# Kernel tuning notes

Hardware: AMD Instinct MI355X
Metric: run time of the kernel (lower is better)

## Reference

```python
import jax, jax.numpy as jnp
import numpy as np

H = 4        # no_heads
CH = 32      # per-head hidden (c_hidden)
INF = 1.0e9

def setup_inputs() -> dict:
    key = jax.random.key(0)
    ks = jax.random.split(key, 8)
    B, I, J, C = 1, 256, 256, 128
    s = 0.02
    return {
        "x": jax.random.normal(ks[0], (B, I, J, C), jnp.float32),
        "mask": jnp.ones((B, I, J), jnp.float32),
        "chunk_size": 0,
        "ln_w": jnp.ones((C,), jnp.float32),
        "ln_b": jnp.zeros((C,), jnp.float32),
        "w_tri": jax.random.normal(ks[1], (C, H), jnp.float32) * s,
        "wq": jax.random.normal(ks[2], (C, H * CH), jnp.float32) * s,
        "wk": jax.random.normal(ks[3], (C, H * CH), jnp.float32) * s,
        "wv": jax.random.normal(ks[4], (C, H * CH), jnp.float32) * s,
        "wg": jax.random.normal(ks[5], (C, H * CH), jnp.float32) * s,
        "bg": jnp.zeros((H * CH,), jnp.float32),
        "wo": jax.random.normal(ks[6], (H * CH, C), jnp.float32) * s,
        "bo": jnp.zeros((C,), jnp.float32),
    }

def _layer_norm(x, w, b, eps=1e-5):
    mu = jnp.mean(x, axis=-1, keepdims=True)
    var = jnp.mean(jnp.square(x - mu), axis=-1, keepdims=True)
    return (x - mu) * jax.lax.rsqrt(var + eps) * w + b

def reference(x, mask, chunk_size, ln_w, ln_b, w_tri, wq, wk, wv, wg, bg, wo, bo):
    # starting=True -> no transpose of (I, J)
    B, I, J, C = x.shape
    xn = _layer_norm(x, ln_w, ln_b)                                   # [B,I,J,C]
    # biases
    mask_bias = (INF * (mask - 1.0))[:, :, None, None, :]             # [B,I,1,1,J]
    tri_bias = jnp.einsum("bijc,ch->bhij", xn, w_tri)[:, None]        # [B,1,H,I,J]
    # gated multi-head attention over the J axis (per row I)
    q = (xn @ wq).reshape(B, I, J, H, CH) * (CH ** -0.5)              # [B,I,J,H,CH]
    k = (xn @ wk).reshape(B, I, J, H, CH)
    v = (xn @ wv).reshape(B, I, J, H, CH)
    scores = jnp.einsum("biqhd,bikhd->bihqk", q, k) + mask_bias + tri_bias
    a = jax.nn.softmax(scores, axis=-1)                               # [B,I,H,J,J]
    o = jnp.einsum("bihqk,bikhd->biqhd", a, v)                        # [B,I,J,H,CH]
    g = jax.nn.sigmoid(xn @ wg + bg).reshape(B, I, J, H, CH)
    o = (o * g).reshape(B, I, J, H * CH)
    return o @ wo + bo                                                # [B,I,J,C]
```

## Files before the change

kernel.cpp:

```cpp
#include <hip/hip_runtime.h>
#include <math.h>

#define NI 256
#define NJ 256
#define NC 128
#define NH 4
#define NCH 32
#define TOKS ((long)NI * NJ)

typedef __attribute__((ext_vector_type(8)))  __bf16        bf16x8;
typedef __attribute__((ext_vector_type(8)))  unsigned short u16x8;
typedef __attribute__((ext_vector_type(4)))  unsigned int   u32x4;
typedef __attribute__((ext_vector_type(16))) float         f32x16;

__device__ __forceinline__ unsigned short f2bf(float f) {
    unsigned u = __builtin_bit_cast(unsigned, f);
    u += 0x7fffu + ((u >> 16) & 1u);
    return (unsigned short)(u >> 16);
}
__device__ __forceinline__ float bf2f(unsigned short s) {
    return __builtin_bit_cast(float, ((unsigned)s) << 16);
}
__device__ __forceinline__ float exp2_fast(float x) {
    float r;
    asm("v_exp_f32 %0, %1" : "=v"(r) : "v"(x));
    return r;
}
__device__ __forceinline__ f32x16 fzero16() {
    f32x16 z;
#pragma unroll
    for (int r = 0; r < 16; ++r) z[r] = 0.f;
    return z;
}
__device__ __forceinline__ f32x16 mfma16(bf16x8 a, bf16x8 b, f32x16 c) {
    return __builtin_amdgcn_mfma_f32_32x32x16_bf16(a, b, c, 0, 0, 0);
}

#define LOG2E 1.4426950408889634f

__global__ __launch_bounds__(256) void convert_weights(
    const float* __restrict__ wq, const float* __restrict__ wk,
    const float* __restrict__ wv, const float* __restrict__ wg,
    const float* __restrict__ wo, const float* __restrict__ w_tri,
    unsigned short* __restrict__ Wt_all, unsigned short* __restrict__ Wto,
    unsigned short* __restrict__ Wtri_pad)
{
    int id = blockIdx.x * 256 + threadIdx.x;
    if (id < 4 * 16384) {
        int m = id >> 14, r = id & 16383;
        int kk = r >> 7, c = r & 127;
        const float* W = (m == 0) ? wq : (m == 1) ? wk : (m == 2) ? wv : wg;
        Wt_all[(m * 128 + c) * 128 + kk] = f2bf(W[kk * 128 + c]);
    } else if (id < 5 * 16384) {
        int r = id - 4 * 16384;
        int kk = r >> 7, c = r & 127;
        Wto[c * 128 + kk] = f2bf(wo[kk * 128 + c]);
    } else {
        int r = id - 5 * 16384;
        int col = r >> 7, kk = r & 127;
        Wtri_pad[col * 128 + kk] = (col < NH) ? f2bf(w_tri[kk * NH + col] * LOG2E)
                                              : (unsigned short)0;
    }
}

#define XNP 136
__global__ __launch_bounds__(256, 2) void ln_proj_mfma(
    const float* __restrict__ x, const float* __restrict__ ln_w, const float* __restrict__ ln_b,
    const unsigned short* __restrict__ Wt_all, const unsigned short* __restrict__ Wtri_pad,
    const float* __restrict__ bg,
    unsigned short* __restrict__ q, unsigned short* __restrict__ k,
    unsigned short* __restrict__ v, unsigned short* __restrict__ g,
    float* __restrict__ tswz)
{
    __shared__ unsigned short xn[64 * XNP];
    const int tid = threadIdx.x;
    const long tok0 = (long)blockIdx.x * 64;

    const int lane8 = tid & 7;
#pragma unroll
    for (int p = 0; p < 2; ++p) {
        const int t = p * 32 + (tid >> 3);
        const float4* xrow = (const float4*)(x + (tok0 + t) * NC + lane8 * 16);
        float4 xv[4];
        float s = 0.f;
#pragma unroll
        for (int u = 0; u < 4; ++u) {
            xv[u] = xrow[u];
            s += xv[u].x + xv[u].y + xv[u].z + xv[u].w;
        }
#pragma unroll
        for (int off = 4; off; off >>= 1) s += __shfl_down(s, off, 8);
        const float mu = __shfl(s, 0, 8) * (1.f / (float)NC);
        float s2 = 0.f;
#pragma unroll
        for (int u = 0; u < 4; ++u) {
            float dx;
            dx = xv[u].x - mu; s2 += dx * dx;
            dx = xv[u].y - mu; s2 += dx * dx;
            dx = xv[u].z - mu; s2 += dx * dx;
            dx = xv[u].w - mu; s2 += dx * dx;
        }
#pragma unroll
        for (int off = 4; off; off >>= 1) s2 += __shfl_down(s2, off, 8);
        const float rstd = rsqrtf(__shfl(s2, 0, 8) * (1.f / (float)NC) + 1e-5f);
#pragma unroll
        for (int u = 0; u < 4; ++u) {
            const int c = lane8 * 16 + u * 4;
            const float4 lw = *(const float4*)(ln_w + c);
            const float4 lb = *(const float4*)(ln_b + c);
            float o0 = (xv[u].x - mu) * rstd * lw.x + lb.x;
            float o1 = (xv[u].y - mu) * rstd * lw.y + lb.y;
            float o2 = (xv[u].z - mu) * rstd * lw.z + lb.z;
            float o3 = (xv[u].w - mu) * rstd * lw.w + lb.w;
            unsigned p0 = (unsigned)f2bf(o0) | ((unsigned)f2bf(o1) << 16);
            unsigned p1 = (unsigned)f2bf(o2) | ((unsigned)f2bf(o3) << 16);
            *(unsigned*)&xn[t * XNP + c]     = p0;
            *(unsigned*)&xn[t * XNP + c + 2] = p1;
        }
    }
    __syncthreads();

    const int w = tid >> 6, L = tid & 63, lh = L >> 5, lc = L & 31;
    f32x16 acc[2][4], accT[2];
#pragma unroll
    for (int mt = 0; mt < 2; ++mt) {
        accT[mt] = fzero16();
#pragma unroll
        for (int nt = 0; nt < 4; ++nt) acc[mt][nt] = fzero16();
    }

#pragma unroll
    for (int k0 = 0; k0 < 8; ++k0) {
        bf16x8 a0 = *(const bf16x8*)&xn[(lc)      * XNP + k0 * 16 + lh * 8];
        bf16x8 a1 = *(const bf16x8*)&xn[(32 + lc) * XNP + k0 * 16 + lh * 8];
#pragma unroll
        for (int nt = 0; nt < 4; ++nt) {
            const int ntile = w + 4 * nt;
            bf16x8 b = *(const bf16x8*)&Wt_all[(ntile * 32 + lc) * 128 + k0 * 16 + lh * 8];
            acc[0][nt] = mfma16(a0, b, acc[0][nt]);
            acc[1][nt] = mfma16(a1, b, acc[1][nt]);
        }
        bf16x8 bt = *(const bf16x8*)&Wtri_pad[lc * 128 + k0 * 16 + lh * 8];
        accT[0] = mfma16(a0, bt, accT[0]);
        accT[1] = mfma16(a1, bt, accT[1]);
    }

    const int a_row = (int)(tok0 >> 8);
    const int b0    = (int)(tok0 & 255);
    int rowl[16];
#pragma unroll
    for (int r = 0; r < 16; ++r) rowl[r] = (r & 3) + 8 * (r >> 2) + 4 * lh;

    if (lc < NH) {
        const int qt_i = a_row >> 5;
        const int lsw  = ((a_row & 31) + 32 * lh) * 16;
#pragma unroll
        for (int mt = 0; mt < 2; ++mt) {
            float* dst = tswz + ((long)((lc * 8 + qt_i) * 8 + (b0 >> 5) + mt)) * 1024 + lsw;
#pragma unroll
            for (int u = 0; u < 4; ++u)
                *(float4*)(dst + u * 4) = make_float4(accT[mt][4*u],   accT[mt][4*u+1],
                                                      accT[mt][4*u+2], accT[mt][4*u+3]);
        }
    }

    const float bgv = bg[w * 32 + lc];
#pragma unroll
    for (int nt = 0; nt < 4; ++nt) {
        unsigned short* O = (nt == 0) ? q : (nt == 1) ? k : (nt == 2) ? v : g;
        __syncthreads();
#pragma unroll
        for (int mt = 0; mt < 2; ++mt) {
#pragma unroll
            for (int r = 0; r < 16; ++r) {
                const int row = mt * 32 + rowl[r];
                float val = acc[mt][nt][r];
                if (nt == 0) val *= 0.25503486f;
                if (nt == 3) val = __builtin_amdgcn_rcpf(1.f + __expf(-(val + bgv)));
                xn[row * XNP + w * 32 + lc] = f2bf(val);
            }
        }
        __syncthreads();
#pragma unroll
        for (int it = 0; it < 4; ++it) {
            const int row = tid >> 2, cc = (tid & 3) * 8;
            *(u16x8*)(O + (((long)a_row * NH + it) * NJ + b0 + row) * NCH + cc) =
                *(const u16x8*)&xn[row * XNP + it * 32 + cc];
        }
    }
}

#define KSP 40
#define VTP 264
#define OSP 36
__global__ __launch_bounds__(256, 2) void attn_fused(
    const unsigned short* __restrict__ q, const unsigned short* __restrict__ k,
    const unsigned short* __restrict__ v, const unsigned short* __restrict__ g,
    const float* __restrict__ tswz, const float* __restrict__ mask,
    const unsigned short* __restrict__ Wto, const float* __restrict__ bo,
    float* __restrict__ out)
{
    __shared__ char smem[75776];
    float* maskb = (float*)(smem + 74752);
    float* outs  = (float*)smem;

    const int i = blockIdx.x, qh = blockIdx.y;
    const int tid = threadIdx.x;
    const int w = tid >> 6, L = tid & 63, lh = L >> 5, lc = L & 31;
    const int qt = qh * 4 + w;
    const int qrow = qt * 32 + lc;

    maskb[tid] = (1.0e9f * LOG2E) * (mask[i * NJ + tid] - 1.0f);

    bf16x8 kreg[4];
    u16x8  vreg[4];
    {
        const long base0 = (long)i * NH * NJ * NCH;
#pragma unroll
        for (int it = 0; it < 4; ++it) {
            const int idx = it * 256 + tid;
            const int key = idx >> 2, c8 = (idx & 3) * 8;
            kreg[it] = *(const bf16x8*)(k + base0 + key * NCH + c8);
        }
#pragma unroll
        for (int u = 0; u < 4; ++u)
            vreg[u] = *(const u16x8*)(v + base0 + (long)tid * NCH + u * 8);
    }

    f32x16 outacc[4];
#pragma unroll
    for (int ct = 0; ct < 4; ++ct) outacc[ct] = fzero16();

#pragma unroll
    for (int h = 0; h < NH; ++h) {
        unsigned short* Ks = (unsigned short*)(smem + (h & 1) * 20480);
        unsigned short* Vt = (unsigned short*)(smem + 40960 + (h & 1) * 16896);
        const long base = ((long)i * NH + h) * NJ * NCH;

        if (h) __syncthreads();
#pragma unroll
        for (int it = 0; it < 4; ++it) {
            const int idx = it * 256 + tid;
            const int key = idx >> 2, c8 = (idx & 3) * 8;
            *(bf16x8*)&Ks[key * KSP + c8] = kreg[it];
        }
#pragma unroll
        for (int u = 0; u < 8; ++u) {
            Vt[(u)      * VTP + tid] = vreg[0][u];
            Vt[(u + 8)  * VTP + tid] = vreg[1][u];
            Vt[(u + 16) * VTP + tid] = vreg[2][u];
            Vt[(u + 24) * VTP + tid] = vreg[3][u];
        }
        __syncthreads();

        if (h < NH - 1) {
            const long basen = base + (long)NJ * NCH;
#pragma unroll
            for (int it = 0; it < 4; ++it) {
                const int idx = it * 256 + tid;
                const int key = idx >> 2, c8 = (idx & 3) * 8;
                kreg[it] = *(const bf16x8*)(k + basen + key * NCH + c8);
            }
#pragma unroll
            for (int u = 0; u < 4; ++u)
                vreg[u] = *(const u16x8*)(v + basen + (long)tid * NCH + u * 8);
        }

        const bf16x8 a0 = *(const bf16x8*)(q + base + (long)qrow * NCH + lh * 8);
        const bf16x8 a1 = *(const bf16x8*)(q + base + (long)qrow * NCH + 16 + lh * 8);
        ushort4 gv[4];
#pragma unroll
        for (int gg = 0; gg < 4; ++gg)
            gv[gg] = *(const ushort4*)(g + base + (long)qrow * NCH + gg * 8 + 4 * lh);
        const float* tbase = tswz + ((long)(h * 8 + qt) * 8) * 1024 + (long)L * 16;

        float ls = 0.f;
        f32x16 O = fzero16();

#pragma unroll
        for (int t = 0; t < 8; ++t) {
            bf16x8 kb0 = *(const bf16x8*)&Ks[(t * 32 + lc) * KSP + lh * 8];
            bf16x8 kb1 = *(const bf16x8*)&Ks[(t * 32 + lc) * KSP + 16 + lh * 8];
            f32x16 s = fzero16();
            s = mfma16(kb0, a0, s);
            s = mfma16(kb1, a1, s);

            unsigned pk[8];
            const float* tv = tbase + (long)t * 1024;
#pragma unroll
            for (int gg = 0; gg < 4; ++gg) {
                const float4 tb = *(const float4*)(tv + gg * 4);
                const float4 mb = *(const float4*)&maskb[t * 32 + gg * 8 + 4 * lh];
                const float p0 = exp2_fast(fminf(s[4 * gg + 0] + tb.x + mb.x, 43.4f));
                const float p1 = exp2_fast(fminf(s[4 * gg + 1] + tb.y + mb.y, 43.4f));
                const float p2 = exp2_fast(fminf(s[4 * gg + 2] + tb.z + mb.z, 43.4f));
                const float p3 = exp2_fast(fminf(s[4 * gg + 3] + tb.w + mb.w, 43.4f));
                ls += (p0 + p1) + (p2 + p3);
                pk[2 * gg]     = (unsigned)f2bf(p0) | ((unsigned)f2bf(p1) << 16);
                pk[2 * gg + 1] = (unsigned)f2bf(p2) | ((unsigned)f2bf(p3) << 16);
            }

#pragma unroll
            for (int ss = 0; ss < 2; ++ss) {
                const unsigned give0 = lh ? pk[4 * ss]     : pk[4 * ss + 2];
                const unsigned give1 = lh ? pk[4 * ss + 1] : pk[4 * ss + 3];
                const unsigned t0 = __shfl_xor(give0, 32);
                const unsigned t1 = __shfl_xor(give1, 32);
                u32x4 bw;
                bw[0] = lh ? t0 : pk[4 * ss];
                bw[1] = lh ? t1 : pk[4 * ss + 1];
                bw[2] = lh ? pk[4 * ss + 2] : t0;
                bw[3] = lh ? pk[4 * ss + 3] : t1;
                const bf16x8 pb = __builtin_bit_cast(bf16x8, bw);
                const bf16x8 va = *(const bf16x8*)&Vt[lc * VTP + t * 32 + ss * 16 + lh * 8];
                O = mfma16(va, pb, O);
            }
        }

        ls += __shfl_xor(ls, 32);
        const float rl = __builtin_amdgcn_rcpf(ls);
        unsigned pk2[8];
#pragma unroll
        for (int gg = 0; gg < 4; ++gg) {
            const float o0 = O[4 * gg + 0] * rl * bf2f(gv[gg].x);
            const float o1 = O[4 * gg + 1] * rl * bf2f(gv[gg].y);
            const float o2 = O[4 * gg + 2] * rl * bf2f(gv[gg].z);
            const float o3 = O[4 * gg + 3] * rl * bf2f(gv[gg].w);
            pk2[2 * gg]     = (unsigned)f2bf(o0) | ((unsigned)f2bf(o1) << 16);
            pk2[2 * gg + 1] = (unsigned)f2bf(o2) | ((unsigned)f2bf(o3) << 16);
        }

#pragma unroll
        for (int ss = 0; ss < 2; ++ss) {
            const unsigned give0 = lh ? pk2[4 * ss]     : pk2[4 * ss + 2];
            const unsigned give1 = lh ? pk2[4 * ss + 1] : pk2[4 * ss + 3];
            const unsigned t0 = __shfl_xor(give0, 32);
            const unsigned t1 = __shfl_xor(give1, 32);
            u32x4 bw;
            bw[0] = lh ? t0 : pk2[4 * ss];
            bw[1] = lh ? t1 : pk2[4 * ss + 1];
            bw[2] = lh ? pk2[4 * ss + 2] : t0;
            bw[3] = lh ? pk2[4 * ss + 3] : t1;
            const bf16x8 ogb = __builtin_bit_cast(bf16x8, bw);
#pragma unroll
            for (int ct = 0; ct < 4; ++ct) {
                const bf16x8 wa = *(const bf16x8*)&Wto[(ct * 32 + lc) * 128 + h * 32 + ss * 16 + lh * 8];
                outacc[ct] = mfma16(wa, ogb, outacc[ct]);
            }
        }
    }

    int rowl[16];
#pragma unroll
    for (int r = 0; r < 16; ++r) rowl[r] = (r & 3) + 8 * (r >> 2) + 4 * lh;
#pragma unroll
    for (int ct = 0; ct < 4; ++ct) {
        __syncthreads();
#pragma unroll
        for (int r = 0; r < 16; ++r)
            outs[(w * 32 + lc) * OSP + rowl[r]] = outacc[ct][r];
        __syncthreads();
#pragma unroll
        for (int it = 0; it < 4; ++it) {
            const int fi = it * 256 + tid;
            const int row = fi >> 3, c4 = fi & 7;
            const float4 vv = *(const float4*)&outs[row * OSP + c4 * 4];
            const float4 bo4 = *(const float4*)(bo + ct * 32 + c4 * 4);
            float4 st;
            st.x = vv.x + bo4.x; st.y = vv.y + bo4.y;
            st.z = vv.z + bo4.z; st.w = vv.w + bo4.w;
            *(float4*)(out + ((long)i * NJ + qh * 128 + row) * NC + ct * 32 + c4 * 4) = st;
        }
    }
}

extern "C" void kernel_launch(void* const* d_in, const int* in_sizes, int n_in,
                              void* d_out, int out_size, void* d_ws, size_t ws_size,
                              hipStream_t stream) {
    const float* x     = (const float*)d_in[0];
    const float* mask  = (const float*)d_in[1];
    const float* ln_w  = (const float*)d_in[3];
    const float* ln_b  = (const float*)d_in[4];
    const float* w_tri = (const float*)d_in[5];
    const float* wq    = (const float*)d_in[6];
    const float* wk    = (const float*)d_in[7];
    const float* wv    = (const float*)d_in[8];
    const float* wg    = (const float*)d_in[9];
    const float* bg    = (const float*)d_in[10];
    const float* wo    = (const float*)d_in[11];
    const float* bo    = (const float*)d_in[12];
    float* out = (float*)d_out;

    char* p = (char*)d_ws;
    const long QB  = TOKS * NC * sizeof(unsigned short);
    unsigned short* q  = (unsigned short*)p; p += QB;
    unsigned short* k  = (unsigned short*)p; p += QB;
    unsigned short* v  = (unsigned short*)p; p += QB;
    unsigned short* g  = (unsigned short*)p; p += QB;
    float* tswz = (float*)p; p += (long)NH * NI * NJ * sizeof(float);
    unsigned short* Wt_all   = (unsigned short*)p; p += 4 * 128 * 128 * sizeof(unsigned short);
    unsigned short* Wto      = (unsigned short*)p; p += 128 * 128 * sizeof(unsigned short);
    unsigned short* Wtri_pad = (unsigned short*)p; p += 32 * 128 * sizeof(unsigned short);

    hipLaunchKernelGGL(convert_weights, dim3(336), dim3(256), 0, stream,
                       wq, wk, wv, wg, wo, w_tri, Wt_all, Wto, Wtri_pad);
    hipLaunchKernelGGL(ln_proj_mfma, dim3(TOKS / 64), dim3(256), 0, stream,
                       x, ln_w, ln_b, Wt_all, Wtri_pad, bg, q, k, v, g, tswz);
    hipLaunchKernelGGL(attn_fused, dim3(NI, 2), dim3(256), 0, stream,
                       q, k, v, g, tswz, mask, Wto, bo, out);
}
```

Measured before the change: 173.2 us.

## Process two heads per pass in attention kernel and use permlane32 swaps

The attention kernel now stages K/V for two heads at once into both shared-memory buffers and interleaves their QK, softmax and PV MFMA chains. This halves the number of block barriers and gives the scheduler independent work to hide MFMA and exp latency. The cross-half shuffles via __shfl_xor are replaced with v_permlane32_swap_b32 inline asm, including the row-sum reduction. The cost is higher register pressure from double K/V prefetch registers and two accumulators, which could spill or cut occupancy under launch_bounds(256,2).

```diff
diff --git a/kernel.cpp b/kernel.cpp
--- a/kernel.cpp
+++ b/kernel.cpp
@@ -25,6 +25,12 @@
     float r;
     asm("v_exp_f32 %0, %1" : "=v"(r) : "v"(x));
     return r;
+}
+__device__ __forceinline__ void permswap(unsigned &a, unsigned &b) {
+    asm volatile("v_permlane32_swap_b32 %0, %1" : "+v"(a), "+v"(b));
+}
+__device__ __forceinline__ void permswapf(float &a, float &b) {
+    asm volatile("v_permlane32_swap_b32 %0, %1" : "+v"(a), "+v"(b));
 }
 __device__ __forceinline__ f32x16 fzero16() {
     f32x16 z;
@@ -201,6 +207,10 @@
     float* __restrict__ out)
 {
     __shared__ char smem[75776];
+    unsigned short* Ks0 = (unsigned short*)smem;
+    unsigned short* Ks1 = (unsigned short*)(smem + 20480);
+    unsigned short* Vt0 = (unsigned short*)(smem + 40960);
+    unsigned short* Vt1 = (unsigned short*)(smem + 40960 + 16896);
     float* maskb = (float*)(smem + 74752);
     float* outs  = (float*)smem;
 
@@ -212,142 +222,177 @@
 
     maskb[tid] = (1.0e9f * LOG2E) * (mask[i * NJ + tid] - 1.0f);
 
-    bf16x8 kreg[4];
-    u16x8  vreg[4];
-    {
-        const long base0 = (long)i * NH * NJ * NCH;
+    const int kidx = tid >> 2, kc8 = (tid & 3) * 8;
+    const long rowbase = (long)i * NH * NJ * NCH;
+
+    bf16x8 kregA[4], kregB[4];
+    u16x8  vregA[4], vregB[4];
+#pragma unroll
+    for (int it = 0; it < 4; ++it) {
+        const int idx = it * 256 + tid;
+        const int key = idx >> 2, c8 = (idx & 3) * 8;
+        kregA[it] = *(const bf16x8*)(k + rowbase + key * NCH + c8);
+        kregB[it] = *(const bf16x8*)(k + rowbase + (long)NJ * NCH + key * NCH + c8);
+    }
+#pragma unroll
+    for (int u = 0; u < 4; ++u) {
+        vregA[u] = *(const u16x8*)(v + rowbase + (long)tid * NCH + u * 8);
+        vregB[u] = *(const u16x8*)(v + rowbase + (long)NJ * NCH + (long)tid * NCH + u * 8);
+    }
+
+    f32x16 outacc[4];
+#pragma unroll
+    for (int ct = 0; ct < 4; ++ct) outacc[ct] = fzero16();
+
+#pragma unroll
+    for (int hp = 0; hp < 2; ++hp) {
+        const int h0 = 2 * hp, h1 = 2 * hp + 1;
+        const long baseA = ((long)i * NH + h0) * NJ * NCH;
+        const long baseB = ((long)i * NH + h1) * NJ * NCH;
+
 #pragma unroll
         for (int it = 0; it < 4; ++it) {
             const int idx = it * 256 + tid;
             const int key = idx >> 2, c8 = (idx & 3) * 8;
-            kreg[it] = *(const bf16x8*)(k + base0 + key * NCH + c8);
-        }
-#pragma unroll
-        for (int u = 0; u < 4; ++u)
-            vreg[u] = *(const u16x8*)(v + base0 + (long)tid * NCH + u * 8);
-    }
-
-    f32x16 outacc[4];
-#pragma unroll
-    for (int ct = 0; ct < 4; ++ct) outacc[ct] = fzero16();
-
-#pragma unroll
-    for (int h = 0; h < NH; ++h) {
-        unsigned short* Ks = (unsigned short*)(smem + (h & 1) * 20480);
-        unsigned short* Vt = (unsigned short*)(smem + 40960 + (h & 1) * 16896);
-        const long base = ((long)i * NH + h) * NJ * NCH;
-
-        if (h) __syncthreads();
-#pragma unroll
-        for (int it = 0; it < 4; ++it) {
-            const int idx = it * 256 + tid;
-            const int key = idx >> 2, c8 = (idx & 3) * 8;
-            *(bf16x8*)&Ks[key * KSP + c8] = kreg[it];
+            *(bf16x8*)&Ks0[key * KSP + c8] = kregA[it];
+            *(bf16x8*)&Ks1[key * KSP + c8] = kregB[it];
         }
 #pragma unroll
         for (int u = 0; u < 8; ++u) {
-            Vt[(u)      * VTP + tid] = vreg[0][u];
-            Vt[(u + 8)  * VTP + tid] = vreg[1][u];
-            Vt[(u + 16) * VTP + tid] = vreg[2][u];
-            Vt[(u + 24) * VTP + tid] = vreg[3][u];
-        }
+            Vt0[(u)      * VTP + tid] = vregA[0][u];
+            Vt0[(u + 8)  * VTP + tid] = vregA[1][u];
+            Vt0[(u + 16) * VTP + tid] = vregA[2][u];
+            Vt0[(u + 24) * VTP + tid] = vregA[3][u];
+            Vt1[(u)      * VTP + tid] = vregB[0][u];
+            Vt1[(u + 8)  * VTP + tid] = vregB[1][u];
+            Vt1[(u + 16) * VTP + tid] = vregB[2][u];
+            Vt1[(u + 24) * VTP + tid] = vregB[3][u];
+        }
+
+        const bf16x8 aA0 = *(const bf16x8*)(q + baseA + (long)qrow * NCH + lh * 8);
+        const bf16x8 aA1 = *(const bf16x8*)(q + baseA + (long)qrow * NCH + 16 + lh * 8);
+        const bf16x8 aB0 = *(const bf16x8*)(q + baseB + (long)qrow * NCH + lh * 8);
+        const bf16x8 aB1 = *(const bf16x8*)(q + baseB + (long)qrow * NCH + 16 + lh * 8);
+        const float* tbA = tswz + ((long)(h0 * 8 + qt) * 8) * 1024 + (long)L * 16;
+        const float* tbB = tswz + ((long)(h1 * 8 + qt) * 8) * 1024 + (long)L * 16;
+
         __syncthreads();
 
-        if (h < NH - 1) {
-            const long basen = base + (long)NJ * NCH;
+        float lsA = 0.f, lsB = 0.f;
+        f32x16 O0 = fzero16(), O1 = fzero16();
+
+#pragma unroll
+        for (int t = 0; t < 8; ++t) {
+            const int krow = (t * 32 + lc) * KSP;
+            bf16x8 ka0 = *(const bf16x8*)&Ks0[krow + lh * 8];
+            bf16x8 ka1 = *(const bf16x8*)&Ks0[krow + 16 + lh * 8];
+            bf16x8 kb0 = *(const bf16x8*)&Ks1[krow + lh * 8];
+            bf16x8 kb1 = *(const bf16x8*)&Ks1[krow + 16 + lh * 8];
+            f32x16 s0 = fzero16(), s1 = fzero16();
+            s0 = mfma16(ka0, aA0, s0);
+            s1 = mfma16(kb0, aB0, s1);
+            s0 = mfma16(ka1, aA1, s0);
+            s1 = mfma16(kb1, aB1, s1);
+
+            unsigned pkA[8], pkB[8];
+            const float* tvA = tbA + (long)t * 1024;
+            const float* tvB = tbB + (long)t * 1024;
+#pragma unroll
+            for (int gg = 0; gg < 4; ++gg) {
+                const float4 mb  = *(const float4*)&maskb[t * 32 + gg * 8 + 4 * lh];
+                const float4 tba = *(const float4*)(tvA + gg * 4);
+                const float4 tbb = *(const float4*)(tvB + gg * 4);
+                const float a0 = exp2_fast(fminf(s0[4*gg+0] + tba.x + mb.x, 43.4f));
+                const float a1 = exp2_fast(fminf(s0[4*gg+1] + tba.y + mb.y, 43.4f));
+                const float a2 = exp2_fast(fminf(s0[4*gg+2] + tba.z + mb.z, 43.4f));
+                const float a3 = exp2_fast(fminf(s0[4*gg+3] + tba.w + mb.w, 43.4f));
+                const float b0_ = exp2_fast(fminf(s1[4*gg+0] + tbb.x + mb.x, 43.4f));
+                const float b1_ = exp2_fast(fminf(s1[4*gg+1] + tbb.y + mb.y, 43.4f));
+                const float b2_ = exp2_fast(fminf(s1[4*gg+2] + tbb.z + mb.z, 43.4f));
+                const float b3_ = exp2_fast(fminf(s1[4*gg+3] + tbb.w + mb.w, 43.4f));
+                lsA += (a0 + a1) + (a2 + a3);
+                lsB += (b0_ + b1_) + (b2_ + b3_);
+                pkA[2*gg]   = (unsigned)f2bf(a0)  | ((unsigned)f2bf(a1)  << 16);
+                pkA[2*gg+1] = (unsigned)f2bf(a2)  | ((unsigned)f2bf(a3)  << 16);
+                pkB[2*gg]   = (unsigned)f2bf(b0_) | ((unsigned)f2bf(b1_) << 16);
+                pkB[2*gg+1] = (unsigned)f2bf(b2_) | ((unsigned)f2bf(b3_) << 16);
+            }
+
+#pragma unroll
+            for (int ss = 0; ss < 2; ++ss) {
+                unsigned x0 = pkA[4*ss], x1 = pkA[4*ss+1], x2 = pkA[4*ss+2], x3 = pkA[4*ss+3];
+                permswap(x0, x2); permswap(x1, x3);
+                u32x4 bwA; bwA[0] = x0; bwA[1] = x1; bwA[2] = x2; bwA[3] = x3;
+                const bf16x8 pbA = __builtin_bit_cast(bf16x8, bwA);
+                const bf16x8 vaA = *(const bf16x8*)&Vt0[lc * VTP + t * 32 + ss * 16 + lh * 8];
+                O0 = mfma16(vaA, pbA, O0);
+
+                unsigned y0 = pkB[4*ss], y1 = pkB[4*ss+1], y2 = pkB[4*ss+2], y3 = pkB[4*ss+3];
+                permswap(y0, y2); permswap(y1, y3);
+                u32x4 bwB; bwB[0] = y0; bwB[1] = y1; bwB[2] = y2; bwB[3] = y3;
+                const bf16x8 pbB = __builtin_bit_cast(bf16x8, bwB);
+                const bf16x8 vaB = *(const bf16x8*)&Vt1[lc * VTP + t * 32 + ss * 16 + lh * 8];
+                O1 = mfma16(vaB, pbB, O1);
+            }
+        }
+
+        if (hp == 0) {
+            const long nA = rowbase + 2L * NJ * NCH;
+            const long nB = rowbase + 3L * NJ * NCH;
 #pragma unroll
             for (int it = 0; it < 4; ++it) {
                 const int idx = it * 256 + tid;
                 const int key = idx >> 2, c8 = (idx & 3) * 8;
-                kreg[it] = *(const bf16x8*)(k + basen + key * NCH + c8);
-            }
-#pragma unroll
-            for (int u = 0; u < 4; ++u)
-                vreg[u] = *(const u16x8*)(v + basen + (long)tid * NCH + u * 8);
-        }
-
-        const bf16x8 a0 = *(const bf16x8*)(q + base + (long)qrow * NCH + lh * 8);
-        const bf16x8 a1 = *(const bf16x8*)(q + base + (long)qrow * NCH + 16 + lh * 8);
-        ushort4 gv[4];
-#pragma unroll
-        for (int gg = 0; gg < 4; ++gg)
-            gv[gg] = *(const ushort4*)(g + base + (long)qrow * NCH + gg * 8 + 4 * lh);
-        const float* tbase = tswz + ((long)(h * 8 + qt) * 8) * 1024 + (long)L * 16;
-
-        float ls = 0.f;
-        f32x16 O = fzero16();
-
-#pragma unroll
-        for (int t = 0; t < 8; ++t) {
-            bf16x8 kb0 = *(const bf16x8*)&Ks[(t * 32 + lc) * KSP + lh * 8];
-            bf16x8 kb1 = *(const bf16x8*)&Ks[(t * 32 + lc) * KSP + 16 + lh * 8];
-            f32x16 s = fzero16();
-            s = mfma16(kb0, a0, s);
-            s = mfma16(kb1, a1, s);
-
-            unsigned pk[8];
-            const float* tv = tbase + (long)t * 1024;
+                kregA[it] = *(const bf16x8*)(k + nA + key * NCH + c8);
+                kregB[it] = *(const bf16x8*)(k + nB + key * NCH + c8);
+            }
+#pragma unroll
+            for (int u = 0; u < 4; ++u) {
+                vregA[u] = *(const u16x8*)(v + nA + (long)tid * NCH + u * 8);
+                vregB[u] = *(const u16x8*)(v + nB + (long)tid * NCH + u * 8);
+            }
+        }
+
+#pragma unroll
+        for (int hs = 0; hs < 2; ++hs) {
+            const long base = hs ? baseB : baseA;
+            const int h = hs ? h1 : h0;
+            f32x16& O = hs ? O1 : O0;
+            float la = hs ? lsB : lsA, lb = la;
+            permswapf(la, lb);
+            const float rl = __builtin_amdgcn_rcpf(la + lb);
+
+            ushort4 gv[4];
+#pragma unroll
+            for (int gg = 0; gg < 4; ++gg)
+                gv[gg] = *(const ushort4*)(g + base + (long)qrow * NCH + gg * 8 + 4 * lh);
+
+            unsigned pk2[8];
 #pragma unroll
             for (int gg = 0; gg < 4; ++gg) {
-                const float4 tb = *(const float4*)(tv + gg * 4);
-                const float4 mb = *(const float4*)&maskb[t * 32 + gg * 8 + 4 * lh];
-                const float p0 = exp2_fast(fminf(s[4 * gg + 0] + tb.x + mb.x, 43.4f));
-                const float p1 = exp2_fast(fminf(s[4 * gg + 1] + tb.y + mb.y, 43.4f));
-                const float p2 = exp2_fast(fminf(s[4 * gg + 2] + tb.z + mb.z, 43.4f));
-                const float p3 = exp2_fast(fminf(s[4 * gg + 3] + tb.w + mb.w, 43.4f));
-                ls += (p0 + p1) + (p2 + p3);
-                pk[2 * gg]     = (unsigned)f2bf(p0) | ((unsigned)f2bf(p1) << 16);
-                pk[2 * gg + 1] = (unsigned)f2bf(p2) | ((unsigned)f2bf(p3) << 16);
+                const float o0 = O[4*gg+0] * rl * bf2f(gv[gg].x);
+                const float o1 = O[4*gg+1] * rl * bf2f(gv[gg].y);
+                const float o2 = O[4*gg+2] * rl * bf2f(gv[gg].z);
+                const float o3 = O[4*gg+3] * rl * bf2f(gv[gg].w);
+                pk2[2*gg]   = (unsigned)f2bf(o0) | ((unsigned)f2bf(o1) << 16);
+                pk2[2*gg+1] = (unsigned)f2bf(o2) | ((unsigned)f2bf(o3) << 16);
             }
 
 #pragma unroll
             for (int ss = 0; ss < 2; ++ss) {
-                const unsigned give0 = lh ? pk[4 * ss]     : pk[4 * ss + 2];
-                const unsigned give1 = lh ? pk[4 * ss + 1] : pk[4 * ss + 3];
-                const unsigned t0 = __shfl_xor(give0, 32);
-                const unsigned t1 = __shfl_xor(give1, 32);
-                u32x4 bw;
-                bw[0] = lh ? t0 : pk[4 * ss];
-                bw[1] = lh ? t1 : pk[4 * ss + 1];
-                bw[2] = lh ? pk[4 * ss + 2] : t0;
-                bw[3] = lh ? pk[4 * ss + 3] : t1;
-                const bf16x8 pb = __builtin_bit_cast(bf16x8, bw);
-                const bf16x8 va = *(const bf16x8*)&Vt[lc * VTP + t * 32 + ss * 16 + lh * 8];
-                O = mfma16(va, pb, O);
-            }
-        }
-
-        ls += __shfl_xor(ls, 32);
-        const float rl = __builtin_amdgcn_rcpf(ls);
-        unsigned pk2[8];
-#pragma unroll
-        for (int gg = 0; gg < 4; ++gg) {
-            const float o0 = O[4 * gg + 0] * rl * bf2f(gv[gg].x);
-            const float o1 = O[4 * gg + 1] * rl * bf2f(gv[gg].y);
-            const float o2 = O[4 * gg + 2] * rl * bf2f(gv[gg].z);
-            const float o3 = O[4 * gg + 3] * rl * bf2f(gv[gg].w);
-            pk2[2 * gg]     = (unsigned)f2bf(o0) | ((unsigned)f2bf(o1) << 16);
-            pk2[2 * gg + 1] = (unsigned)f2bf(o2) | ((unsigned)f2bf(o3) << 16);
-        }
-
-#pragma unroll
-        for (int ss = 0; ss < 2; ++ss) {
-            const unsigned give0 = lh ? pk2[4 * ss]     : pk2[4 * ss + 2];
-            const unsigned give1 = lh ? pk2[4 * ss + 1] : pk2[4 * ss + 3];
-            const unsigned t0 = __shfl_xor(give0, 32);
-            const unsigned t1 = __shfl_xor(give1, 32);
-            u32x4 bw;
-            bw[0] = lh ? t0 : pk2[4 * ss];
-            bw[1] = lh ? t1 : pk2[4 * ss + 1];
-            bw[2] = lh ? pk2[4 * ss + 2] : t0;
-            bw[3] = lh ? pk2[4 * ss + 3] : t1;
-            const bf16x8 ogb = __builtin_bit_cast(bf16x8, bw);
-#pragma unroll
-            for (int ct = 0; ct < 4; ++ct) {
-                const bf16x8 wa = *(const bf16x8*)&Wto[(ct * 32 + lc) * 128 + h * 32 + ss * 16 + lh * 8];
-                outacc[ct] = mfma16(wa, ogb, outacc[ct]);
-            }
-        }
+                unsigned x0 = pk2[4*ss], x1 = pk2[4*ss+1], x2 = pk2[4*ss+2], x3 = pk2[4*ss+3];
+                permswap(x0, x2); permswap(x1, x3);
+                u32x4 bw; bw[0] = x0; bw[1] = x1; bw[2] = x2; bw[3] = x3;
+                const bf16x8 ogb = __builtin_bit_cast(bf16x8, bw);
+#pragma unroll
+                for (int ct = 0; ct < 4; ++ct) {
+                    const bf16x8 wa = *(const bf16x8*)&Wto[(ct * 32 + lc) * 128 + h * 32 + ss * 16 + lh * 8];
+                    outacc[ct] = mfma16(wa, ogb, outacc[ct]);
+                }
+            }
+        }
+
+        if (hp == 0) __syncthreads();
     }
 
     int rowl[16];
```

Result: slower. 214.0 us (+23.6%).
